# Optimization experiments

Hardware: AMD Instinct MI355X
Metric: run time of the kernel (lower is better)

## Reference

```python
import jax, jax.numpy as jnp
import numpy as np

BATCH = 512          # bs_large + bs_small
COMBINED_BS = 320    # bs_large + bs_small // (r_large // r_small)
R = 64               # r_large
K = 4096             # hidden dim, fixed in the TIR kernel
N_ADAPT = 80         # combined adapters


def setup_inputs() -> dict:
    key = jax.random.key(0)
    k1, k2, k3, k4 = jax.random.split(key, 4)
    x = jax.random.normal(k1, (BATCH, 1, K), dtype=jnp.float32)
    xids = jax.random.randint(k2, (COMBINED_BS * R,), 0, BATCH, dtype=jnp.int32)
    wids = jax.random.randint(k3, (COMBINED_BS,), 0, N_ADAPT, dtype=jnp.int32)
    A = jax.random.normal(k4, (N_ADAPT, K, R), dtype=jnp.float32) * 0.02
    return {"x": x, "xids": xids, "wids": wids, "A": A}


def reference(x, xids, wids, A):
    # out[c, 0, r] = sum_k x[xids[c*R + r], 0, k] * A[wids[c], k, r]
    C = wids.shape[0]
    r = A.shape[2]
    tok = xids.reshape(C, r)          # per-output-element token ids
    xg = x[tok, 0, :]                 # (C, R, K) gathered activations
    Ag = A[wids]                      # (C, K, R) gathered adapters
    out = jnp.einsum('crk,ckr->cr', xg, Ag)
    return out[:, None, :]            # (C, 1, R)
```

## Files before the change

kernel.cpp:

```cpp
#include <hip/hip_runtime.h>
#include <stdint.h>

namespace {
constexpr int BATCH  = 512;
constexpr int CBS    = 320;
constexpr int R      = 64;
constexpr int K      = 4096;
constexpr int NADAPT = 80;
constexpr int SPLIT  = 8;
constexpr int KS     = K / SPLIT;
constexpr int TK     = 128;
constexpr int NT     = 256;
constexpr int NW     = NT / 64;
constexpr int NPH    = KS / TK;
constexpr int G      = 4;
constexpr int MAXG   = (CBS + (G - 1) * NADAPT) / G;

constexpr size_t WS_XB_OFF = 8192;
constexpr size_t WS_NEEDED = WS_XB_OFF + (size_t)BATCH * K * 2;

__device__ inline uint16_t f2bf(float f) {
    uint32_t u = __float_as_uint(f);
    u += 0x7fffu + ((u >> 16) & 1u);
    return (uint16_t)(u >> 16);
}
__device__ inline float bflo(uint32_t u) { return __uint_as_float(u << 16); }
__device__ inline float bfhi(uint32_t u) { return __uint_as_float(u & 0xffff0000u); }
}

__global__ void groups_build(const int* __restrict__ wids,
                             int* __restrict__ gcnt, int* __restrict__ gwid,
                             int* __restrict__ gc)
{
    __shared__ int hist[NADAPT];
    __shared__ int offs[NADAPT];
    __shared__ int gbase[NADAPT];
    const int t = threadIdx.x;
    if (t < NADAPT) { hist[t] = 0; offs[t] = 0; }
    if (t < MAXG) gcnt[t] = 0;
    __syncthreads();
    atomicAdd(&hist[wids[t]], 1);
    __syncthreads();
    if (t == 0) {
        int run = 0;
        for (int w = 0; w < NADAPT; ++w) { gbase[w] = run; run += (hist[w] + G - 1) / G; }
    }
    __syncthreads();
    const int w   = wids[t];
    const int rk  = atomicAdd(&offs[w], 1);
    const int gid = gbase[w] + (rk >> 2);
    gc[gid * G + (rk & 3)] = t;
    gwid[gid] = w;
    atomicAdd(&gcnt[gid], 1);
}

__global__ __launch_bounds__(256)
void cvt_x(const float* __restrict__ x, uint16_t* __restrict__ xb)
{
    const int i = blockIdx.x * 256 + threadIdx.x;
    const float4 v = ((const float4*)x)[i];
    ushort4 o;
    o.x = f2bf(v.x); o.y = f2bf(v.y); o.z = f2bf(v.z); o.w = f2bf(v.w);
    ((ushort4*)xb)[i] = o;
}

__global__ __launch_bounds__(NT, 2)
void lora_main(const int* __restrict__ xids,
               const float* __restrict__ A,
               const uint16_t* __restrict__ xb,
               const int* __restrict__ gcnt, const int* __restrict__ gwid,
               const int* __restrict__ gc,
               float* __restrict__ out)
{
    __shared__ uint32_t xs[G * (TK / 2) * R];
    __shared__ float red[G * NW * R];

    const int bid = blockIdx.x;
    const int gid = bid >> 3;
    const int s   = bid & 7;
    const int cnt = gcnt[gid];
    if (cnt == 0) return;
    const int wid = gwid[gid];
    const float* __restrict__ Aw = A + (size_t)wid * (K * R);

    const int t    = threadIdx.x;
    const int wave = t >> 6;
    const int lane = t & 63;
    const int r4   = lane & 15;
    const int kq   = lane >> 4;
    const int rw   = t >> 2;
    const int jq   = t & 3;
    const int rsw  = rw ^ (jq << 4);

    const uint16_t* __restrict__ xrow[G];
#pragma unroll
    for (int g = 0; g < G; ++g) {
        const int c   = (g < cnt) ? gc[gid * G + g] : gc[gid * G];
        const int tok = xids[c * R + rw];
        xrow[g] = xb + (size_t)tok * K + s * KS + jq * 32;
    }

    float4 acc[G];
#pragma unroll
    for (int g = 0; g < G; ++g) acc[g] = make_float4(0.f, 0.f, 0.f, 0.f);

    const int rr = (4 * r4) ^ (wave << 4);

    for (int ph = 0; ph < NPH; ++ph) {
#pragma unroll
        for (int g = 0; g < G; ++g) {
            if (g < cnt) {
                const uint4* src = (const uint4*)(xrow[g] + ph * TK);
                uint4 u0 = src[0], u1 = src[1], u2 = src[2], u3 = src[3];
                uint32_t* dst = &xs[g * (TK / 2) * R + (jq * 16) * R + rsw];
                dst[ 0 * R] = u0.x; dst[ 1 * R] = u0.y; dst[ 2 * R] = u0.z; dst[ 3 * R] = u0.w;
                dst[ 4 * R] = u1.x; dst[ 5 * R] = u1.y; dst[ 6 * R] = u1.z; dst[ 7 * R] = u1.w;
                dst[ 8 * R] = u2.x; dst[ 9 * R] = u2.y; dst[10 * R] = u2.z; dst[11 * R] = u2.w;
                dst[12 * R] = u3.x; dst[13 * R] = u3.y; dst[14 * R] = u3.z; dst[15 * R] = u3.w;
            }
        }
        __syncthreads();

#pragma unroll
        for (int i = 0; i < 4; ++i) {
            const int p  = wave * 16 + i * 4 + kq;
            const int k0 = s * KS + ph * TK + 2 * p;
            const float* __restrict__ Ap = Aw + (size_t)k0 * R + 4 * r4;
            const float4 a0 = *(const float4*)(Ap);
            const float4 a1 = *(const float4*)(Ap + R);
#pragma unroll
            for (int g = 0; g < G; ++g) {
                if (g < cnt) {
                    const uint4 f = *(const uint4*)&xs[g * (TK / 2) * R + p * R + rr];
                    acc[g].x = fmaf(bflo(f.x), a0.x, acc[g].x);
                    acc[g].y = fmaf(bflo(f.y), a0.y, acc[g].y);
                    acc[g].z = fmaf(bflo(f.z), a0.z, acc[g].z);
                    acc[g].w = fmaf(bflo(f.w), a0.w, acc[g].w);
                    acc[g].x = fmaf(bfhi(f.x), a1.x, acc[g].x);
                    acc[g].y = fmaf(bfhi(f.y), a1.y, acc[g].y);
                    acc[g].z = fmaf(bfhi(f.z), a1.z, acc[g].z);
                    acc[g].w = fmaf(bfhi(f.w), a1.w, acc[g].w);
                }
            }
        }
        __syncthreads();
    }

#pragma unroll
    for (int g = 0; g < G; ++g) {
#pragma unroll
        for (int m = 16; m < 64; m <<= 1) {
            acc[g].x += __shfl_xor(acc[g].x, m, 64);
            acc[g].y += __shfl_xor(acc[g].y, m, 64);
            acc[g].z += __shfl_xor(acc[g].z, m, 64);
            acc[g].w += __shfl_xor(acc[g].w, m, 64);
        }
    }
    if (kq == 0) {
#pragma unroll
        for (int g = 0; g < G; ++g)
            *(float4*)&red[(g * NW + wave) * R + 4 * r4] = acc[g];
    }
    __syncthreads();
    {
        const int g = wave;
        if (g < cnt) {
            const int c = gc[gid * G + g];
            const float sum = red[(g * NW + 0) * R + lane] + red[(g * NW + 1) * R + lane]
                            + red[(g * NW + 2) * R + lane] + red[(g * NW + 3) * R + lane];
            atomicAdd(&out[c * R + lane], sum);
        }
    }
}

__global__ __launch_bounds__(NT)
void lora_fallback(const float* __restrict__ x,
                   const int*   __restrict__ xids,
                   const int*   __restrict__ wids,
                   const float* __restrict__ A,
                   float*       __restrict__ out)
{
    __shared__ float xsf[64 * R];
    __shared__ float red[NW * R];
    const int bid  = blockIdx.x;
    const int c    = bid >> 3;
    const int s    = bid & 7;
    const int t    = threadIdx.x;
    const int wave = t >> 6;
    const int lane = t & 63;
    const int r4   = lane & 15;
    const int kq   = lane >> 4;
    const int wid  = wids[c];
    const float* __restrict__ Aw = A + (size_t)wid * (K * R);
    const int rw  = t >> 2;
    const int jq  = t & 3;
    const int tok = xids[c * R + rw];
    const float* __restrict__ xrow = x + (size_t)tok * K + s * KS + jq * 16;
    float4 acc = make_float4(0.f, 0.f, 0.f, 0.f);
    for (int tile = 0; tile < KS / 64; ++tile) {
        const float4* src = (const float4*)(xrow + tile * 64);
#pragma unroll
        for (int ii = 0; ii < 4; ++ii) {
            float4 v = src[ii];
            const int kk = jq * 16 + ii * 4;
            xsf[(kk + 0) * R + rw] = v.x;
            xsf[(kk + 1) * R + rw] = v.y;
            xsf[(kk + 2) * R + rw] = v.z;
            xsf[(kk + 3) * R + rw] = v.w;
        }
        __syncthreads();
        const int kw = wave * 16 + kq;
        const float* __restrict__ Ap =
            Aw + (size_t)(s * KS + tile * 64 + kw) * R + 4 * r4;
#pragma unroll
        for (int i = 0; i < 4; ++i) {
            float4 av = *(const float4*)(Ap + (size_t)(4 * i) * R);
            float4 xv = *(const float4*)(&xsf[(kw + 4 * i) * R + 4 * r4]);
            acc.x = fmaf(xv.x, av.x, acc.x);
            acc.y = fmaf(xv.y, av.y, acc.y);
            acc.z = fmaf(xv.z, av.z, acc.z);
            acc.w = fmaf(xv.w, av.w, acc.w);
        }
        __syncthreads();
    }
#pragma unroll
    for (int m = 16; m < 64; m <<= 1) {
        acc.x += __shfl_xor(acc.x, m, 64);
        acc.y += __shfl_xor(acc.y, m, 64);
        acc.z += __shfl_xor(acc.z, m, 64);
        acc.w += __shfl_xor(acc.w, m, 64);
    }
    if (kq == 0) {
        float* rd = &red[wave * R + 4 * r4];
        rd[0] = acc.x; rd[1] = acc.y; rd[2] = acc.z; rd[3] = acc.w;
    }
    __syncthreads();
    if (wave == 0) {
        float sum = red[lane] + red[R + lane] + red[2 * R + lane] + red[3 * R + lane];
        atomicAdd(&out[c * R + lane], sum);
    }
}

extern "C" void kernel_launch(void* const* d_in, const int* in_sizes, int n_in,
                              void* d_out, int out_size, void* d_ws, size_t ws_size,
                              hipStream_t stream)
{
    (void)in_sizes; (void)n_in;
    const float* x    = (const float*)d_in[0];
    const int*   xids = (const int*)d_in[1];
    const int*   wids = (const int*)d_in[2];
    const float* A    = (const float*)d_in[3];
    float* out        = (float*)d_out;

    hipMemsetAsync(out, 0, (size_t)out_size * sizeof(float), stream);

    if (ws_size >= WS_NEEDED) {
        int*      wsi  = (int*)d_ws;
        int*      gcnt = wsi;
        int*      gwid = wsi + 256;
        int*      gc   = wsi + 512;
        uint16_t* xb   = (uint16_t*)((char*)d_ws + WS_XB_OFF);
        hipLaunchKernelGGL(groups_build, dim3(1), dim3(CBS), 0, stream,
                           wids, gcnt, gwid, gc);
        hipLaunchKernelGGL(cvt_x, dim3(BATCH * K / 4 / 256), dim3(256), 0, stream, x, xb);
        hipLaunchKernelGGL(lora_main, dim3(MAXG * SPLIT), dim3(NT), 0, stream,
                           xids, A, xb, gcnt, gwid, gc, out);
    } else {
        hipLaunchKernelGGL(lora_fallback, dim3(CBS * SPLIT), dim3(NT), 0, stream,
                           x, xids, wids, A, out);
    }
}
```

Baseline: 160.3 us.

## Fold adapter grouping into main kernel and register-prefetch next x tile

Drops the separate single-block groups_build launch. Each main-kernel block now recomputes the adapter histogram and its own group membership in shared memory, using an O(CBS) rank scan per thread. The K tile shrinks from 128 to 64, and the next tile's bf16 activations are prefetched into registers while the current tile is computed, to overlap global loads with FMAs. The min-blocks launch bound is removed. This trades one kernel launch and its dependency for redundant per-block setup work, and may raise register pressure.

```diff
diff --git a/kernel.cpp b/kernel.cpp
--- a/kernel.cpp
+++ b/kernel.cpp
@@ -9,15 +9,16 @@
 constexpr int NADAPT = 80;
 constexpr int SPLIT  = 8;
 constexpr int KS     = K / SPLIT;
-constexpr int TK     = 128;
+constexpr int TK     = 64;
+constexpr int NTILES = KS / TK;
 constexpr int NT     = 256;
 constexpr int NW     = NT / 64;
-constexpr int NPH    = KS / TK;
 constexpr int G      = 4;
 constexpr int MAXG   = (CBS + (G - 1) * NADAPT) / G;
-
-constexpr size_t WS_XB_OFF = 8192;
-constexpr size_t WS_NEEDED = WS_XB_OFF + (size_t)BATCH * K * 2;
+constexpr int NBLK   = MAXG * SPLIT;
+
+constexpr size_t WS_XB_OFF = 0;
+constexpr size_t WS_NEEDED = (size_t)BATCH * K * 2;
 
 __device__ inline uint16_t f2bf(float f) {
     uint32_t u = __float_as_uint(f);
@@ -26,32 +27,6 @@
 }
 __device__ inline float bflo(uint32_t u) { return __uint_as_float(u << 16); }
 __device__ inline float bfhi(uint32_t u) { return __uint_as_float(u & 0xffff0000u); }
-}
-
-__global__ void groups_build(const int* __restrict__ wids,
-                             int* __restrict__ gcnt, int* __restrict__ gwid,
-                             int* __restrict__ gc)
-{
-    __shared__ int hist[NADAPT];
-    __shared__ int offs[NADAPT];
-    __shared__ int gbase[NADAPT];
-    const int t = threadIdx.x;
-    if (t < NADAPT) { hist[t] = 0; offs[t] = 0; }
-    if (t < MAXG) gcnt[t] = 0;
-    __syncthreads();
-    atomicAdd(&hist[wids[t]], 1);
-    __syncthreads();
-    if (t == 0) {
-        int run = 0;
-        for (int w = 0; w < NADAPT; ++w) { gbase[w] = run; run += (hist[w] + G - 1) / G; }
-    }
-    __syncthreads();
-    const int w   = wids[t];
-    const int rk  = atomicAdd(&offs[w], 1);
-    const int gid = gbase[w] + (rk >> 2);
-    gc[gid * G + (rk & 3)] = t;
-    gwid[gid] = w;
-    atomicAdd(&gcnt[gid], 1);
 }
 
 __global__ __launch_bounds__(256)
@@ -64,26 +39,52 @@
     ((ushort4*)xb)[i] = o;
 }
 
-__global__ __launch_bounds__(NT, 2)
+__global__ __launch_bounds__(NT)
 void lora_main(const int* __restrict__ xids,
+               const int* __restrict__ wids,
                const float* __restrict__ A,
                const uint16_t* __restrict__ xb,
-               const int* __restrict__ gcnt, const int* __restrict__ gwid,
-               const int* __restrict__ gc,
                float* __restrict__ out)
 {
+    __shared__ int swids[CBS];
+    __shared__ int hist[NADAPT];
+    __shared__ int gmem[G];
+    __shared__ int meta[2];
     __shared__ uint32_t xs[G * (TK / 2) * R];
     __shared__ float red[G * NW * R];
 
-    const int bid = blockIdx.x;
-    const int gid = bid >> 3;
-    const int s   = bid & 7;
-    const int cnt = gcnt[gid];
-    if (cnt == 0) return;
-    const int wid = gwid[gid];
-    const float* __restrict__ Aw = A + (size_t)wid * (K * R);
-
-    const int t    = threadIdx.x;
+    const int t      = threadIdx.x;
+    const int my_gid = blockIdx.x >> 3;
+    const int s      = blockIdx.x & 7;
+
+    for (int i = t; i < CBS; i += NT) swids[i] = wids[i];
+    if (t < NADAPT) hist[t] = 0;
+    if (t == 0) meta[0] = -1;
+    __syncthreads();
+    for (int i = t; i < CBS; i += NT) atomicAdd(&hist[swids[i]], 1);
+    __syncthreads();
+    if (t == 0) {
+        int run = 0;
+        for (int w = 0; w < NADAPT; ++w) {
+            const int gb = run;
+            run += (hist[w] + G - 1) >> 2;
+            if (my_gid >= gb && my_gid < run) { meta[0] = w; meta[1] = (my_gid - gb) << 2; }
+        }
+    }
+    __syncthreads();
+    const int wid = meta[0];
+    if (wid < 0) return;
+    const int base_rank = meta[1];
+    const int cnt = min(G, hist[wid] - base_rank);
+    for (int i = t; i < CBS; i += NT) {
+        if (swids[i] == wid) {
+            int rk = 0;
+            for (int j = 0; j < i; ++j) rk += (swids[j] == wid) ? 1 : 0;
+            if (rk >= base_rank && rk < base_rank + G) gmem[rk - base_rank] = i;
+        }
+    }
+    __syncthreads();
+
     const int wave = t >> 6;
     const int lane = t & 63;
     const int r4   = lane & 15;
@@ -92,39 +93,52 @@
     const int jq   = t & 3;
     const int rsw  = rw ^ (jq << 4);
 
-    const uint16_t* __restrict__ xrow[G];
+    const float* __restrict__ Aw = A + (size_t)wid * (K * R);
+
+    int cidx[G];
+    const uint4* __restrict__ xrow[G];
 #pragma unroll
     for (int g = 0; g < G; ++g) {
-        const int c   = (g < cnt) ? gc[gid * G + g] : gc[gid * G];
-        const int tok = xids[c * R + rw];
-        xrow[g] = xb + (size_t)tok * K + s * KS + jq * 32;
+        cidx[g] = (g < cnt) ? gmem[g] : gmem[0];
+        const int tok = xids[cidx[g] * R + rw];
+        xrow[g] = (const uint4*)(xb + (size_t)tok * K + s * KS + jq * 16);
     }
 
     float4 acc[G];
 #pragma unroll
     for (int g = 0; g < G; ++g) acc[g] = make_float4(0.f, 0.f, 0.f, 0.f);
 
+    uint4 p0[G], p1[G];
+#pragma unroll
+    for (int g = 0; g < G; ++g)
+        if (g < cnt) { p0[g] = xrow[g][0]; p1[g] = xrow[g][1]; }
+
     const int rr = (4 * r4) ^ (wave << 4);
 
-    for (int ph = 0; ph < NPH; ++ph) {
+    for (int tile = 0; tile < NTILES; ++tile) {
 #pragma unroll
         for (int g = 0; g < G; ++g) {
             if (g < cnt) {
-                const uint4* src = (const uint4*)(xrow[g] + ph * TK);
-                uint4 u0 = src[0], u1 = src[1], u2 = src[2], u3 = src[3];
-                uint32_t* dst = &xs[g * (TK / 2) * R + (jq * 16) * R + rsw];
-                dst[ 0 * R] = u0.x; dst[ 1 * R] = u0.y; dst[ 2 * R] = u0.z; dst[ 3 * R] = u0.w;
-                dst[ 4 * R] = u1.x; dst[ 5 * R] = u1.y; dst[ 6 * R] = u1.z; dst[ 7 * R] = u1.w;
-                dst[ 8 * R] = u2.x; dst[ 9 * R] = u2.y; dst[10 * R] = u2.z; dst[11 * R] = u2.w;
-                dst[12 * R] = u3.x; dst[13 * R] = u3.y; dst[14 * R] = u3.z; dst[15 * R] = u3.w;
+                uint32_t* dst = &xs[g * (TK / 2) * R + (jq * 8) * R + rsw];
+                dst[0 * R] = p0[g].x; dst[1 * R] = p0[g].y;
+                dst[2 * R] = p0[g].z; dst[3 * R] = p0[g].w;
+                dst[4 * R] = p1[g].x; dst[5 * R] = p1[g].y;
+                dst[6 * R] = p1[g].z; dst[7 * R] = p1[g].w;
             }
         }
         __syncthreads();
 
-#pragma unroll
-        for (int i = 0; i < 4; ++i) {
-            const int p  = wave * 16 + i * 4 + kq;
-            const int k0 = s * KS + ph * TK + 2 * p;
+        if (tile + 1 < NTILES) {
+            const int off = (tile + 1) * (TK / 2 / 4);
+#pragma unroll
+            for (int g = 0; g < G; ++g)
+                if (g < cnt) { p0[g] = xrow[g][off]; p1[g] = xrow[g][off + 1]; }
+        }
+
+#pragma unroll
+        for (int i = 0; i < 2; ++i) {
+            const int p  = wave * 8 + i * 4 + kq;
+            const int k0 = s * KS + tile * TK + 2 * p;
             const float* __restrict__ Ap = Aw + (size_t)k0 * R + 4 * r4;
             const float4 a0 = *(const float4*)(Ap);
             const float4 a1 = *(const float4*)(Ap + R);
@@ -165,10 +179,9 @@
     {
         const int g = wave;
         if (g < cnt) {
-            const int c = gc[gid * G + g];
             const float sum = red[(g * NW + 0) * R + lane] + red[(g * NW + 1) * R + lane]
                             + red[(g * NW + 2) * R + lane] + red[(g * NW + 3) * R + lane];
-            atomicAdd(&out[c * R + lane], sum);
+            atomicAdd(&out[gmem[g] * R + lane], sum);
         }
     }
 }
@@ -184,7 +197,7 @@
     __shared__ float red[NW * R];
     const int bid  = blockIdx.x;
     const int c    = bid >> 3;
-    const int s    = bid & 7;
+    const int sl   = bid & 7;
     const int t    = threadIdx.x;
     const int wave = t >> 6;
     const int lane = t & 63;
@@ -195,7 +208,7 @@
     const int rw  = t >> 2;
     const int jq  = t & 3;
     const int tok = xids[c * R + rw];
-    const float* __restrict__ xrow = x + (size_t)tok * K + s * KS + jq * 16;
+    const float* __restrict__ xrow = x + (size_t)tok * K + sl * KS + jq * 16;
     float4 acc = make_float4(0.f, 0.f, 0.f, 0.f);
     for (int tile = 0; tile < KS / 64; ++tile) {
         const float4* src = (const float4*)(xrow + tile * 64);
@@ -211,7 +224,7 @@
         __syncthreads();
         const int kw = wave * 16 + kq;
         const float* __restrict__ Ap =
-            Aw + (size_t)(s * KS + tile * 64 + kw) * R + 4 * r4;
+            Aw + (size_t)(sl * KS + tile * 64 + kw) * R + 4 * r4;
 #pragma unroll
         for (int i = 0; i < 4; ++i) {
             float4 av = *(const float4*)(Ap + (size_t)(4 * i) * R);
@@ -255,16 +268,10 @@
     hipMemsetAsync(out, 0, (size_t)out_size * sizeof(float), stream);
 
     if (ws_size >= WS_NEEDED) {
-        int*      wsi  = (int*)d_ws;
-        int*      gcnt = wsi;
-        int*      gwid = wsi + 256;
-        int*      gc   = wsi + 512;
-        uint16_t* xb   = (uint16_t*)((char*)d_ws + WS_XB_OFF);
-        hipLaunchKernelGGL(groups_build, dim3(1), dim3(CBS), 0, stream,
-                           wids, gcnt, gwid, gc);
+        uint16_t* xb = (uint16_t*)((char*)d_ws + WS_XB_OFF);
         hipLaunchKernelGGL(cvt_x, dim3(BATCH * K / 4 / 256), dim3(256), 0, stream, x, xb);
-        hipLaunchKernelGGL(lora_main, dim3(MAXG * SPLIT), dim3(NT), 0, stream,
-                           xids, A, xb, gcnt, gwid, gc, out);
+        hipLaunchKernelGGL(lora_main, dim3(NBLK), dim3(NT), 0, stream,
+                           xids, wids, A, xb, out);
     } else {
         hipLaunchKernelGGL(lora_fallback, dim3(CBS * SPLIT), dim3(NT), 0, stream,
                            x, xids, wids, A, out);
```

New measurement: 161.5 us. About the same (+0.7%).
